# Kernel tuning notes

Measured on AMD Instinct MI355X. Metric: run time of the kernel, lower is better.

## Reference

```python
import jax, jax.numpy as jnp
import numpy as np

RARITY_ALPHA = 0.5


def _forward(obs_emb, observed_mask, lengths, avg_interval, var_prior_emb_tensor,
             rarity_W, adjI, p2s_W1, p2s_b1, p2s_W2, p2s_b2,
             Wu, bu, Wr, br, Wc, bc):
    B, T, N, D = obs_emb.shape
    I = jnp.eye(N, dtype=obs_emb.dtype)
    # hypernetwork conditioning vector per node (prior_to_state MLP); identical
    # across batch since var_prior_emb_tensor is repeated over the batch dim.
    vv = jax.nn.relu(var_prior_emb_tensor @ p2s_W1 + p2s_b1) @ p2s_W2 + p2s_b2  # [N,E]
    vv = jnp.broadcast_to(vv[None], (B, N, vv.shape[-1]))                        # [B,N,E]
    tot = observed_mask.sum(axis=1)  # var_total_obs [B,N]

    def gate(z, W, b):
        # MLP_Param: per-node weights W_n = sum_e vv[n,e]*W[e]; fused einsum avoids
        # materializing [B,N,2D+1,D].
        return jnp.einsum('bni,bne,eio->bno', z, vv, W) + jnp.einsum('bne,eo->bno', vv, b)

    def step_fn(carry, xs):
        h, out = carry
        cur_obs, m, cur_avg, step = xs  # [B,N,D], [B,N], [B,N], scalar
        rs = RARITY_ALPHA * jnp.tanh(cur_avg / (tot + 1.0))                  # [B,N]
        rmat = -rarity_W * jnp.abs(rs[:, :, None] - rs[:, None, :])          # [B,N,N]
        # adj_mask[b,i,j] = observed(b,i)*observed(b,j)  (column-set then row-zero)
        adj_mask = m[:, :, None] * m[:, None, :]
        cur_adj = adjI * (1.0 + rmat) * adj_mask * (1.0 - I) + I             # [B,N,N]
        x = jnp.concatenate([cur_obs, rs[..., None]], axis=-1)              # [B,N,D+1]
        comb = jnp.einsum('bij,bjf->bif', cur_adj,
                          jnp.concatenate([x, h], axis=-1))                  # [B,N,2D+1]
        r = jax.nn.sigmoid(gate(comb, Wr, br))
        u = jax.nn.sigmoid(gate(comb, Wu, bu))
        mm = m[..., None] > 0
        h1 = jnp.where(mm, r * h, h)                      # h[nodes_ind] = r*h[nodes_ind]
        cand = jnp.tanh(gate(jnp.concatenate([x, h1], axis=-1), Wc, bc))
        h2 = jnp.where(mm, (1.0 - u) * h1 + u * cand, h1)  # scatter back at observed nodes
        out = jnp.where((step == lengths - 1)[:, None, None], h2, out)
        return (h2, out), None

    h0 = jnp.zeros((B, N, D), obs_emb.dtype)
    xs = (obs_emb.transpose(1, 0, 2, 3), observed_mask.transpose(1, 0, 2),
          avg_interval.transpose(1, 0, 2), jnp.arange(T))
    (_, out), _ = jax.lax.scan(step_fn, (h0, jnp.zeros_like(h0)), xs)
    return out


def setup_inputs() -> dict:
    B, T, N, D, E = 32, 64, 128, 64, 5
    key = jax.random.key(0)
    ks = jax.random.split(key, 18)
    inp = {}
    inp['obs_emb'] = jax.random.normal(ks[0], (B, T, N, D), jnp.float32)
    inp['adj'] = jax.random.normal(ks[1], (N, N), jnp.float32)  # unused by forward
    inp['observed_mask'] = (jax.random.uniform(ks[2], (B, T, N)) < 0.5).astype(jnp.float32)
    inp['observed_tp'] = jax.random.uniform(ks[3], (B, T), jnp.float32)       # unused
    inp['tp_emb_tensor'] = jax.random.normal(ks[4], (B, T, 1), jnp.float32)   # unused
    inp['lengths'] = jax.random.randint(ks[5], (B,), T // 2, T + 1, jnp.int32)
    inp['avg_interval'] = jax.random.uniform(ks[6], (B, T, N), jnp.float32)
    inp['var_prior_emb_tensor'] = jax.random.normal(ks[7], (N, 768), jnp.float32)
    # learned parameters
    inp['rarity_W'] = jax.random.normal(ks[8], (N, N), jnp.float32)
    inp['adjI'] = jnp.eye(N, dtype=jnp.float32) + 0.01 * jax.random.normal(ks[9], (N, N), jnp.float32)
    inp['p2s_W1'] = 0.05 * jax.random.normal(ks[10], (768, 2 * D), jnp.float32)
    inp['p2s_b1'] = jnp.zeros((2 * D,), jnp.float32)
    inp['p2s_W2'] = 0.1 * jax.random.normal(ks[11], (2 * D, E), jnp.float32)
    inp['p2s_b2'] = jnp.zeros((E,), jnp.float32)
    inp['Wu'] = 0.1 * jax.random.normal(ks[12], (E, 2 * D + 1, D), jnp.float32)
    inp['bu'] = 0.1 * jax.random.normal(ks[13], (E, D), jnp.float32)
    inp['Wr'] = 0.1 * jax.random.normal(ks[14], (E, 2 * D + 1, D), jnp.float32)
    inp['br'] = 0.1 * jax.random.normal(ks[15], (E, D), jnp.float32)
    inp['Wc'] = 0.1 * jax.random.normal(ks[16], (E, 2 * D + 1, D), jnp.float32)
    inp['bc'] = 0.1 * jax.random.normal(ks[17], (E, D), jnp.float32)
    return inp


def reference(obs_emb, adj, observed_mask, observed_tp, tp_emb_tensor, lengths,
              avg_interval, var_prior_emb_tensor, rarity_W, adjI, p2s_W1, p2s_b1,
              p2s_W2, p2s_b2, Wu, bu, Wr, br, Wc, bc):
    # adj, observed_tp, tp_emb_tensor are accepted but never used, as in the torch code
    return _forward(obs_emb, observed_mask, lengths, avg_interval, var_prior_emb_tensor,
                    rarity_W, adjI, p2s_W1, p2s_b1, p2s_W2, p2s_b2,
                    Wu, bu, Wr, br, Wc, bc)
```

## Files before the change

### kernel.cpp

```cpp
#include <hip/hip_runtime.h>
#include <math.h>

constexpr size_t WS_VV  = 1024;
constexpr size_t WS_TOT = 2048;
constexpr size_t WS_RS  = 8192;
constexpr size_t WS_WH  = 270336;
constexpr size_t WS_WX  = 1843200;
constexpr size_t WS_BF  = 3440640;
constexpr size_t WS_H   = 3465216;
constexpr size_t WS_CH  = 3727360;
constexpr size_t WS_CX  = 3989504;
constexpr size_t WS_GXR = 8249344;
constexpr size_t WS_GXU = 12443648;
constexpr size_t WS_CXC = 16637952;

__device__ __forceinline__ float sigm(float x){ return 1.f/(1.f+expf(-x)); }

__device__ __forceinline__ float2 ld2_mall(const float* p){
  union { unsigned long long u; float2 f; } cv;
  cv.u = __hip_atomic_load((const unsigned long long*)p, __ATOMIC_RELAXED,
                           __HIP_MEMORY_SCOPE_AGENT);
  return cv.f;
}
__device__ __forceinline__ void st2_mall(float* p, float a, float b){
  union { unsigned long long u; float2 f; } cv;
  cv.f = make_float2(a, b);
  __hip_atomic_store((unsigned long long*)p, cv.u, __ATOMIC_RELAXED,
                     __HIP_MEMORY_SCOPE_AGENT);
}

__global__ void k_vv(const float* __restrict__ vpe, const float* __restrict__ W1,
                     const float* __restrict__ b1, const float* __restrict__ W2,
                     const float* __restrict__ b2, float* __restrict__ ws){
  int n = blockIdx.x, tid = threadIdx.x;
  __shared__ float hid[128];
  if (tid < 128){
    float acc = b1[tid];
    for (int k=0;k<768;k++) acc = fmaf(vpe[n*768+k], W1[k*128+tid], acc);
    hid[tid] = fmaxf(acc, 0.f);
  }
  __syncthreads();
  if (tid < 5){
    float acc = b2[tid];
    for (int h=0;h<128;h++) acc = fmaf(hid[h], W2[h*5+tid], acc);
    ws[WS_VV + n*5 + tid] = acc;
  }
}

__global__ void k_fold(const float* __restrict__ Wr, const float* __restrict__ Wu,
                       const float* __restrict__ Wc, const float* __restrict__ br,
                       const float* __restrict__ bu, const float* __restrict__ bc,
                       float* __restrict__ ws){
  int bid = blockIdx.x; int g = bid>>7; int n = bid&127;
  const float* W  = (g==0)?Wr:(g==1)?Wu:Wc;
  const float* bb = (g==0)?br:(g==1)?bu:bc;
  float v[5];
#pragma unroll
  for (int e=0;e<5;e++) v[e] = ws[WS_VV + n*5 + e];
  for (int idx=threadIdx.x; idx<129*64; idx+=256){
    int i = idx>>6, o = idx&63;
    float a = 0.f;
#pragma unroll
    for (int e=0;e<5;e++) a = fmaf(v[e], W[(e*129+i)*64+o], a);
    if (i < 65) ws[WS_WX + (size_t)(g*128+n)*4160 + i*64 + o] = a;
    else        ws[WS_WH + (size_t)(g*128+n)*4096 + (i-65)*64 + o] = a;
  }
  if (threadIdx.x < 64){
    int o = threadIdx.x; float a = 0.f;
#pragma unroll
    for (int e=0;e<5;e++) a = fmaf(v[e], bb[e*64+o], a);
    ws[WS_BF + (g*128+n)*64 + o] = a;
  }
}

__global__ void k_tot(const float* __restrict__ mask, float* __restrict__ ws){
  int id = blockIdx.x*256 + threadIdx.x;
  int b = id>>7, n = id&127;
  float s = 0.f;
  for (int t=0;t<64;t++) s += mask[(b*64+t)*128 + n];
  ws[WS_TOT + b*128 + n] = s;
}

__global__ void k_rs(const float* __restrict__ avg, float* __restrict__ ws){
  int id = blockIdx.x*256 + threadIdx.x;
  int b = id>>13, n = id&127;
  float tot = ws[WS_TOT + b*128 + n];
  ws[WS_RS + id] = 0.5f * tanhf(avg[id] / (tot + 1.f));
}

__global__ __launch_bounds__(256) void p4a(const float* __restrict__ obs,
      const float* __restrict__ mask, const float* __restrict__ adjI,
      const float* __restrict__ rW, const int* __restrict__ lengths,
      float* __restrict__ ws, int c0){
  int rc = blockIdx.x;
  int b = rc>>4, tl = rc&15, t = c0 + tl;
  if (t >= lengths[b]) return;
  int rt = b*64 + t;
  __shared__ float xt[64*68];
  __shared__ float adjh[128*68];
  __shared__ float rs_l[128], m_l[128];
  int tid = threadIdx.x;
  if (tid < 128){ rs_l[tid] = ws[WS_RS + rt*128 + tid]; m_l[tid] = mask[rt*128 + tid]; }
  __syncthreads();
  int it = tid>>3, ft = tid&7, i0 = it*4, f0 = ft*8;
  float4 aL[4], aH[4]; float a64[4];
#pragma unroll
  for (int ii=0;ii<4;ii++){ aL[ii]=make_float4(0,0,0,0); aH[ii]=make_float4(0,0,0,0); a64[ii]=0.f; }
  for (int half=0; half<2; half++){
    __syncthreads();
    int j0 = half*64;
    for (int idx=tid; idx<4096; idx+=256){
      int jl = idx>>6, f = idx&63;
      xt[jl*68+f] = obs[(size_t)rt*8192 + (j0+jl)*64 + f];
    }
    if (tid < 64) xt[tid*68+64] = rs_l[j0+tid];
    for (int idx=tid; idx<8192; idx+=256){
      int i = idx>>6, jl = idx&63, j = j0+jl;
      float a;
      if (i == j) a = 1.f;
      else {
        int gi = i*128 + j;
        float dd = fabsf(rs_l[i] - rs_l[j]);
        a = adjI[gi] * (1.f - rW[gi]*dd) * m_l[i] * m_l[j];
      }
      adjh[i*68+jl] = a;
    }
    __syncthreads();
    for (int jb=0; jb<16; jb++){
      float4 av[4];
#pragma unroll
      for (int ii=0;ii<4;ii++) av[ii] = *(const float4*)&adjh[(i0+ii)*68 + jb*4];
#pragma unroll
      for (int jj=0;jj<4;jj++){
        int jl = jb*4 + jj;
        float4 xlo = *(const float4*)&xt[jl*68 + f0];
        float4 xhi = *(const float4*)&xt[jl*68 + f0 + 4];
        float xr = xt[jl*68 + 64];
#pragma unroll
        for (int ii=0;ii<4;ii++){
          float a = (jj==0)?av[ii].x:(jj==1)?av[ii].y:(jj==2)?av[ii].z:av[ii].w;
          aL[ii].x = fmaf(a, xlo.x, aL[ii].x); aL[ii].y = fmaf(a, xlo.y, aL[ii].y);
          aL[ii].z = fmaf(a, xlo.z, aL[ii].z); aL[ii].w = fmaf(a, xlo.w, aL[ii].w);
          aH[ii].x = fmaf(a, xhi.x, aH[ii].x); aH[ii].y = fmaf(a, xhi.y, aH[ii].y);
          aH[ii].z = fmaf(a, xhi.z, aH[ii].z); aH[ii].w = fmaf(a, xhi.w, aH[ii].w);
          a64[ii] = fmaf(a, xr, a64[ii]);
        }
      }
    }
  }
#pragma unroll
  for (int ii=0;ii<4;ii++){
    int i = i0 + ii;
    size_t base = WS_CX + (size_t)i*33280 + (size_t)rc*65 + f0;
    ws[base+0]=aL[ii].x; ws[base+1]=aL[ii].y; ws[base+2]=aL[ii].z; ws[base+3]=aL[ii].w;
    ws[base+4]=aH[ii].x; ws[base+5]=aH[ii].y; ws[base+6]=aH[ii].z; ws[base+7]=aH[ii].w;
    if (ft == 0) ws[WS_CX + (size_t)i*33280 + (size_t)rc*65 + 64] = a64[ii];
  }
}

__global__ __launch_bounds__(256) void p4b(const float* __restrict__ obs,
      const int* __restrict__ lengths, float* __restrict__ ws, int c0){
  int bid = blockIdx.x;
  int g = bid >> 9; int r2 = bid & 511; int n = r2 >> 2; int tile = r2 & 3;
  __shared__ float A[128*69];
  __shared__ float Wl[65*64];
  __shared__ float bl[64];
  __shared__ int slen[32];
  int tid = threadIdx.x;
  if (tid < 32) slen[tid] = lengths[tid];
  for (int idx=tid; idx<4160; idx+=256) Wl[idx] = ws[WS_WX + (size_t)(g*128+n)*4160 + idx];
  if (tid < 64) bl[tid] = ws[WS_BF + (g*128+n)*64 + tid];
  if (g < 2){
    const float* src = &ws[WS_CX + (size_t)n*33280 + (size_t)tile*8320];
    for (int idx=tid; idx<8320; idx+=256){
      int r = idx/65, f = idx - r*65;
      A[r*69+f] = src[idx];
    }
  } else {
    for (int idx=tid; idx<8320; idx+=256){
      int r = idx/65, f = idx - r*65;
      int grow = tile*128 + r;
      int gb = grow>>4, t = c0 + (grow&15);
      float v = (f < 64) ? obs[(size_t)(gb*64+t)*8192 + n*64 + f]
                         : ws[WS_RS + (gb*64+t)*128 + n];
      A[r*69+f] = v;
    }
  }
  __syncthreads();
  int rt8 = tid>>4, dq = tid&15;
  float4 acc[8];
#pragma unroll
  for (int rr=0;rr<8;rr++) acc[rr] = make_float4(0,0,0,0);
  for (int k=0;k<65;k++){
    float4 w = *(const float4*)&Wl[k*64 + dq*4];
#pragma unroll
    for (int rr=0;rr<8;rr++){
      float a = A[(rt8*8+rr)*69 + k];
      acc[rr].x = fmaf(a,w.x,acc[rr].x); acc[rr].y = fmaf(a,w.y,acc[rr].y);
      acc[rr].z = fmaf(a,w.z,acc[rr].z); acc[rr].w = fmaf(a,w.w,acc[rr].w);
    }
  }
  float4 b4 = *(const float4*)&bl[dq*4];
  float* dst = &ws[(g==0)?WS_GXR:(g==1)?WS_GXU:WS_CXC];
#pragma unroll
  for (int rr=0;rr<8;rr++){
    int grow = tile*128 + rt8*8 + rr;
    int gb = grow>>4, gtl = grow&15;
    if (c0 + gtl < slen[gb]){
      float4 o; o.x=acc[rr].x+b4.x; o.y=acc[rr].y+b4.y; o.z=acc[rr].z+b4.z; o.w=acc[rr].w+b4.w;
      *(float4*)&dst[((size_t)(n*16+gtl)*32 + gb)*64 + dq*4] = o;
    }
  }
}

__global__ __launch_bounds__(256) void krec(const float* __restrict__ mask,
      const int* __restrict__ lengths, const float* __restrict__ adjI,
      const float* __restrict__ rWm, float* __restrict__ out, float* __restrict__ ws,
      int c0){
  unsigned* hfl = (unsigned*)ws;
  const int bid = blockIdx.x, tid = threadIdx.x;
  const int bA = bid>>3, s = bid&7, ns = s*16;
  __shared__ float hs[8192];
  __shared__ float adjT[2560];
  __shared__ float chT[1088];
  __shared__ float hT[1088];
  __shared__ float rs_l[128], m_l[128];
  const int lenA = lengths[bA];
  const int ng = tid>>6, fA = tid&63;
  const int nl = tid>>4, fq = tid&15;
  const int n  = ns + nl;
  float* hbuf = &ws[WS_H];
  const float* wrg = &ws[WS_WH + (size_t)(0*128+n)*4096];
  const float* wug = &ws[WS_WH + (size_t)(1*128+n)*4096];
  const float* wcg = &ws[WS_WH + (size_t)(2*128+n)*4096];

  for (int t=c0; t<c0+16; t++){
    if (t >= lenA){
      if (tid == 0)
        __hip_atomic_store(&hfl[bid], (unsigned)(t+1), __ATOMIC_RELAXED,
                           __HIP_MEMORY_SCOPE_AGENT);
      __syncthreads();
      continue;
    }
    if (tid < 128) rs_l[tid] = ws[WS_RS + (size_t)(bA*64+t)*128 + tid];
    else           m_l[tid-128] = mask[(size_t)(bA*64+t)*128 + (tid-128)];
    __syncthreads();
    for (int idx=tid; idx<2048; idx+=256){
      int j = idx&127, il = idx>>7, I = ns+il;
      float a;
      if (I == j) a = 1.f;
      else {
        int gi = I*128 + j;
        float dd = fabsf(rs_l[I] - rs_l[j]);
        a = adjI[gi]*(1.f - rWm[gi]*dd)*m_l[I]*m_l[j];
      }
      adjT[j*20 + il] = a;
    }
    const int tl = t - c0;
    size_t gof = ((size_t)(n*16+tl)*32 + bA)*64 + fq*4;
    float4 arv = *(const float4*)&ws[WS_GXR + gof];
    float4 auv = *(const float4*)&ws[WS_GXU + gof];
    float4 acv = *(const float4*)&ws[WS_CXC + gof];
    float  msv = m_l[n];
    if (t > 0){
      if (tid < 8){
        unsigned tgt = (unsigned)t; int guard = 0;
        while (__hip_atomic_load(&hfl[bA*8 + tid], __ATOMIC_RELAXED,
                 __HIP_MEMORY_SCOPE_AGENT) < tgt && ++guard < (1<<20))
          __builtin_amdgcn_s_sleep(2);
      }
    }
    __syncthreads();
#pragma unroll
    for (int k=0;k<16;k++){
      int p = tid + 256*k;
      float2 v = ld2_mall(&hbuf[(size_t)bA*8192 + 2*p]);
      *(float2*)&hs[2*p] = v;
    }
    __syncthreads();
    float acc[4] = {0.f,0.f,0.f,0.f};
#pragma unroll 4
    for (int j=0;j<128;j++){
      float hv = hs[j*64 + fA];
      float4 a4 = *(const float4*)&adjT[j*20 + ng*4];
      acc[0] = fmaf(a4.x, hv, acc[0]);
      acc[1] = fmaf(a4.y, hv, acc[1]);
      acc[2] = fmaf(a4.z, hv, acc[2]);
      acc[3] = fmaf(a4.w, hv, acc[3]);
    }
#pragma unroll
    for (int r=0;r<4;r++) chT[(ng*4+r)*68 + fA] = acc[r];
    __syncthreads();
#pragma unroll 4
    for (int k=0;k<64;k++){
      float cv = chT[nl*68 + k];
      float4 wr4 = *(const float4*)&wrg[k*64 + fq*4];
      float4 wu4 = *(const float4*)&wug[k*64 + fq*4];
      arv.x = fmaf(cv,wr4.x,arv.x); arv.y = fmaf(cv,wr4.y,arv.y);
      arv.z = fmaf(cv,wr4.z,arv.z); arv.w = fmaf(cv,wr4.w,arv.w);
      auv.x = fmaf(cv,wu4.x,auv.x); auv.y = fmaf(cv,wu4.y,auv.y);
      auv.z = fmaf(cv,wu4.z,auv.z); auv.w = fmaf(cv,wu4.w,auv.w);
    }
    float4 rr4, uu4, h1;
    rr4.x = sigm(arv.x); rr4.y = sigm(arv.y); rr4.z = sigm(arv.z); rr4.w = sigm(arv.w);
    uu4.x = sigm(auv.x); uu4.y = sigm(auv.y); uu4.z = sigm(auv.z); uu4.w = sigm(auv.w);
    float4 hown = *(const float4*)&hs[n*64 + fq*4];
    bool ob = msv > 0.f;
    h1.x = ob ? rr4.x*hown.x : hown.x;
    h1.y = ob ? rr4.y*hown.y : hown.y;
    h1.z = ob ? rr4.z*hown.z : hown.z;
    h1.w = ob ? rr4.w*hown.w : hown.w;
    *(float4*)&hT[nl*68 + fq*4] = h1;
    __syncthreads();
#pragma unroll 4
    for (int k=0;k<64;k++){
      float hv1 = hT[nl*68 + k];
      float4 wc4 = *(const float4*)&wcg[k*64 + fq*4];
      acv.x = fmaf(hv1,wc4.x,acv.x); acv.y = fmaf(hv1,wc4.y,acv.y);
      acv.z = fmaf(hv1,wc4.z,acv.z); acv.w = fmaf(hv1,wc4.w,acv.w);
    }
    float4 cd, h2;
    cd.x = tanhf(acv.x); cd.y = tanhf(acv.y); cd.z = tanhf(acv.z); cd.w = tanhf(acv.w);
    h2.x = ob ? (1.f-uu4.x)*h1.x + uu4.x*cd.x : h1.x;
    h2.y = ob ? (1.f-uu4.y)*h1.y + uu4.y*cd.y : h1.y;
    h2.z = ob ? (1.f-uu4.z)*h1.z + uu4.z*cd.z : h1.z;
    h2.w = ob ? (1.f-uu4.w)*h1.w + uu4.w*cd.w : h1.w;
    float* hp = &hbuf[((size_t)bA*128 + n)*64 + fq*4];
    st2_mall(hp,   h2.x, h2.y);
    st2_mall(hp+2, h2.z, h2.w);
    if (t == lenA-1)
      *(float4*)&out[((size_t)bA*128 + n)*64 + fq*4] = h2;
    __syncthreads();
    asm volatile("s_waitcnt vmcnt(0)" ::: "memory");
    if (tid == 0)
      __hip_atomic_store(&hfl[bid], (unsigned)(t+1), __ATOMIC_RELAXED,
                         __HIP_MEMORY_SCOPE_AGENT);
  }
}

extern "C" void kernel_launch(void* const* d_in, const int* in_sizes, int n_in,
                              void* d_out, int out_size, void* d_ws, size_t ws_size,
                              hipStream_t stream){
  const float* obs  = (const float*)d_in[0];
  const float* maskp= (const float*)d_in[2];
  const int*   lens = (const int*)d_in[5];
  const float* avg  = (const float*)d_in[6];
  const float* vpe  = (const float*)d_in[7];
  const float* rW   = (const float*)d_in[8];
  const float* adjI = (const float*)d_in[9];
  const float* W1   = (const float*)d_in[10];
  const float* b1   = (const float*)d_in[11];
  const float* W2   = (const float*)d_in[12];
  const float* b2   = (const float*)d_in[13];
  const float* Wu   = (const float*)d_in[14];
  const float* bu   = (const float*)d_in[15];
  const float* Wr   = (const float*)d_in[16];
  const float* br   = (const float*)d_in[17];
  const float* Wc   = (const float*)d_in[18];
  const float* bc   = (const float*)d_in[19];
  float* out = (float*)d_out;
  float* ws  = (float*)d_ws;
  hipMemsetAsync(d_ws, 0, 4096, stream);
  hipMemsetAsync((char*)d_ws + WS_H*sizeof(float), 0, 262144*sizeof(float), stream);
  k_vv  <<<128, 256, 0, stream>>>(vpe, W1, b1, W2, b2, ws);
  k_fold<<<384, 256, 0, stream>>>(Wr, Wu, Wc, br, bu, bc, ws);
  k_tot <<<16,  256, 0, stream>>>(maskp, ws);
  k_rs  <<<1024,256, 0, stream>>>(avg, ws);
  for (int c = 0; c < 4; c++){
    int c0 = c*16;
    p4a <<<512, 256, 0, stream>>>(obs, maskp, adjI, rW, lens, ws, c0);
    p4b <<<1536,256, 0, stream>>>(obs, lens, ws, c0);
    krec<<<256, 256, 0, stream>>>(maskp, lens, adjI, rW, out, ws, c0);
  }
}
```

Before: 1.528 ms.

## Split recurrent step into batch-major aggregation and node-major gate phases

```diff
diff --git a/kernel.cpp b/kernel.cpp
--- a/kernel.cpp
+++ b/kernel.cpp
@@ -217,123 +217,157 @@
       const int* __restrict__ lengths, const float* __restrict__ adjI,
       const float* __restrict__ rWm, float* __restrict__ out, float* __restrict__ ws,
       int c0){
-  unsigned* hfl = (unsigned*)ws;
+  unsigned* cfl = (unsigned*)ws;
+  unsigned* hfl = ((unsigned*)ws) + 256;
   const int bid = blockIdx.x, tid = threadIdx.x;
-  const int bA = bid>>3, s = bid&7, ns = s*16;
+  const int bA = bid>>3, sA = bid&7, ns = sA*16;
+  const int nB = bid>>1, hf = bid&1, b0 = hf*16;
   __shared__ float hs[8192];
   __shared__ float adjT[2560];
-  __shared__ float chT[1088];
+  __shared__ float cT[1088];
   __shared__ float hT[1088];
   __shared__ float rs_l[128], m_l[128];
   const int lenA = lengths[bA];
-  const int ng = tid>>6, fA = tid&63;
-  const int nl = tid>>4, fq = tid&15;
-  const int n  = ns + nl;
+  const int il = tid>>4, fq = tid&15;
+  const int bb = b0 + il;
+  const int slenB = lengths[bb];
   float* hbuf = &ws[WS_H];
-  const float* wrg = &ws[WS_WH + (size_t)(0*128+n)*4096];
-  const float* wug = &ws[WS_WH + (size_t)(1*128+n)*4096];
-  const float* wcg = &ws[WS_WH + (size_t)(2*128+n)*4096];
+  float* chb  = &ws[WS_CH];
+  const float* wrg = &ws[WS_WH + (size_t)(0*128+nB)*4096];
+  const float* wug = &ws[WS_WH + (size_t)(1*128+nB)*4096];
+  const float* wcg = &ws[WS_WH + (size_t)(2*128+nB)*4096];
+  float4 hst;
+  { const float* hp = &hbuf[((size_t)bb*128+nB)*64 + fq*4];
+    float2 lo = ld2_mall(hp), hi = ld2_mall(hp+2);
+    hst = make_float4(lo.x, lo.y, hi.x, hi.y); }
 
   for (int t=c0; t<c0+16; t++){
-    if (t >= lenA){
-      if (tid == 0)
-        __hip_atomic_store(&hfl[bid], (unsigned)(t+1), __ATOMIC_RELAXED,
-                           __HIP_MEMORY_SCOPE_AGENT);
-      __syncthreads();
-      continue;
-    }
-    if (tid < 128) rs_l[tid] = ws[WS_RS + (size_t)(bA*64+t)*128 + tid];
-    else           m_l[tid-128] = mask[(size_t)(bA*64+t)*128 + (tid-128)];
-    __syncthreads();
-    for (int idx=tid; idx<2048; idx+=256){
-      int j = idx&127, il = idx>>7, I = ns+il;
-      float a;
-      if (I == j) a = 1.f;
-      else {
-        int gi = I*128 + j;
-        float dd = fabsf(rs_l[I] - rs_l[j]);
-        a = adjI[gi]*(1.f - rWm[gi]*dd)*m_l[I]*m_l[j];
-      }
-      adjT[j*20 + il] = a;
-    }
     const int tl = t - c0;
-    size_t gof = ((size_t)(n*16+tl)*32 + bA)*64 + fq*4;
-    float4 arv = *(const float4*)&ws[WS_GXR + gof];
-    float4 auv = *(const float4*)&ws[WS_GXU + gof];
-    float4 acv = *(const float4*)&ws[WS_CXC + gof];
-    float  msv = m_l[n];
-    if (t > 0){
-      if (tid < 8){
-        unsigned tgt = (unsigned)t; int guard = 0;
-        while (__hip_atomic_load(&hfl[bA*8 + tid], __ATOMIC_RELAXED,
-                 __HIP_MEMORY_SCOPE_AGENT) < tgt && ++guard < (1<<20))
-          __builtin_amdgcn_s_sleep(2);
-      }
-    }
-    __syncthreads();
-#pragma unroll
-    for (int k=0;k<16;k++){
-      int p = tid + 256*k;
-      float2 v = ld2_mall(&hbuf[(size_t)bA*8192 + 2*p]);
-      *(float2*)&hs[2*p] = v;
-    }
-    __syncthreads();
-    float acc[4] = {0.f,0.f,0.f,0.f};
+    const bool aliveA = (t < lenA);
+    const bool aliveB = (t < slenB);
+    if (aliveA){
+      if (tid < 128) rs_l[tid] = ws[WS_RS + (size_t)(bA*64+t)*128 + tid];
+      else           m_l[tid-128] = mask[(size_t)(bA*64+t)*128 + (tid-128)];
+    }
+    __syncthreads();
+    if (aliveA){
+      for (int idx=tid; idx<2048; idx+=256){
+        int j = idx&127, r = idx>>7, I = ns+r;
+        float a;
+        if (I == j) a = 1.f;
+        else {
+          int gi = I*128 + j;
+          float dd = fabsf(rs_l[I] - rs_l[j]);
+          a = adjI[gi]*(1.f - rWm[gi]*dd)*m_l[I]*m_l[j];
+        }
+        adjT[j*20 + r] = a;
+      }
+    }
+    float4 arv, auv, acv; float msv = 0.f;
+    if (aliveB){
+      size_t gof = ((size_t)(nB*16+tl)*32 + bb)*64 + fq*4;
+      arv = *(const float4*)&ws[WS_GXR + gof];
+      auv = *(const float4*)&ws[WS_GXU + gof];
+      acv = *(const float4*)&ws[WS_CXC + gof];
+      msv = mask[(size_t)(bb*64+t)*128 + nB];
+    }
+    if (aliveA && t > 0 && tid < 128){
+      unsigned tgt = (unsigned)t; int guard = 0;
+      while (__hip_atomic_load(&hfl[tid*2 + (bA>>4)], __ATOMIC_RELAXED,
+               __HIP_MEMORY_SCOPE_AGENT) < tgt && ++guard < (1<<20))
+        __builtin_amdgcn_s_sleep(1);
+    }
+    __syncthreads();
+    if (aliveA){
+#pragma unroll
+      for (int k2=0;k2<16;k2++){
+        int p = tid + 256*k2;
+        float2 v = ld2_mall(&hbuf[(size_t)bA*8192 + 2*p]);
+        *(float2*)&hs[2*p] = v;
+      }
+    }
+    __syncthreads();
+    if (aliveA && tid < 128){
+      int pr = tid>>4;
+      float4 a0 = make_float4(0,0,0,0), a1 = a0;
 #pragma unroll 4
-    for (int j=0;j<128;j++){
-      float hv = hs[j*64 + fA];
-      float4 a4 = *(const float4*)&adjT[j*20 + ng*4];
-      acc[0] = fmaf(a4.x, hv, acc[0]);
-      acc[1] = fmaf(a4.y, hv, acc[1]);
-      acc[2] = fmaf(a4.z, hv, acc[2]);
-      acc[3] = fmaf(a4.w, hv, acc[3]);
-    }
-#pragma unroll
-    for (int r=0;r<4;r++) chT[(ng*4+r)*68 + fA] = acc[r];
-    __syncthreads();
+      for (int j=0;j<128;j++){
+        float2 aj = *(const float2*)&adjT[j*20 + pr*2];
+        float4 h4 = *(const float4*)&hs[j*64 + fq*4];
+        a0.x = fmaf(aj.x,h4.x,a0.x); a0.y = fmaf(aj.x,h4.y,a0.y);
+        a0.z = fmaf(aj.x,h4.z,a0.z); a0.w = fmaf(aj.x,h4.w,a0.w);
+        a1.x = fmaf(aj.y,h4.x,a1.x); a1.y = fmaf(aj.y,h4.y,a1.y);
+        a1.z = fmaf(aj.y,h4.z,a1.z); a1.w = fmaf(aj.y,h4.w,a1.w);
+      }
+      float* cp0 = &chb[((size_t)bA*128 + ns + pr*2)*64 + fq*4];
+      st2_mall(cp0,    a0.x, a0.y); st2_mall(cp0+2,  a0.z, a0.w);
+      st2_mall(cp0+64, a1.x, a1.y); st2_mall(cp0+66, a1.z, a1.w);
+    }
+    __syncthreads();
+    if (tid == 0)
+      __hip_atomic_store(&cfl[sA*32 + bA], (unsigned)(t+1), __ATOMIC_RELAXED,
+                         __HIP_MEMORY_SCOPE_AGENT);
+    if (aliveB && fq == 0){
+      unsigned tgt = (unsigned)(t+1); int guard = 0;
+      while (__hip_atomic_load(&cfl[(nB>>4)*32 + bb], __ATOMIC_RELAXED,
+               __HIP_MEMORY_SCOPE_AGENT) < tgt && ++guard < (1<<20))
+        __builtin_amdgcn_s_sleep(1);
+    }
+    __syncthreads();
+    if (aliveB){
+      const float* cp = &chb[((size_t)bb*128 + nB)*64 + fq*4];
+      float2 u = ld2_mall(cp), v = ld2_mall(cp+2);
+      cT[il*68 + fq*4    ] = u.x; cT[il*68 + fq*4 + 1] = u.y;
+      cT[il*68 + fq*4 + 2] = v.x; cT[il*68 + fq*4 + 3] = v.y;
+    }
+    __syncthreads();
+    float4 uu, h1v;
+    const bool ob = msv > 0.f;
+    if (aliveB){
 #pragma unroll 4
-    for (int k=0;k<64;k++){
-      float cv = chT[nl*68 + k];
-      float4 wr4 = *(const float4*)&wrg[k*64 + fq*4];
-      float4 wu4 = *(const float4*)&wug[k*64 + fq*4];
-      arv.x = fmaf(cv,wr4.x,arv.x); arv.y = fmaf(cv,wr4.y,arv.y);
-      arv.z = fmaf(cv,wr4.z,arv.z); arv.w = fmaf(cv,wr4.w,arv.w);
-      auv.x = fmaf(cv,wu4.x,auv.x); auv.y = fmaf(cv,wu4.y,auv.y);
-      auv.z = fmaf(cv,wu4.z,auv.z); auv.w = fmaf(cv,wu4.w,auv.w);
-    }
-    float4 rr4, uu4, h1;
-    rr4.x = sigm(arv.x); rr4.y = sigm(arv.y); rr4.z = sigm(arv.z); rr4.w = sigm(arv.w);
-    uu4.x = sigm(auv.x); uu4.y = sigm(auv.y); uu4.z = sigm(auv.z); uu4.w = sigm(auv.w);
-    float4 hown = *(const float4*)&hs[n*64 + fq*4];
-    bool ob = msv > 0.f;
-    h1.x = ob ? rr4.x*hown.x : hown.x;
-    h1.y = ob ? rr4.y*hown.y : hown.y;
-    h1.z = ob ? rr4.z*hown.z : hown.z;
-    h1.w = ob ? rr4.w*hown.w : hown.w;
-    *(float4*)&hT[nl*68 + fq*4] = h1;
-    __syncthreads();
+      for (int k=0;k<64;k++){
+        float cv = cT[il*68 + k];
+        float4 wr4 = *(const float4*)&wrg[k*64 + fq*4];
+        float4 wu4 = *(const float4*)&wug[k*64 + fq*4];
+        arv.x = fmaf(cv,wr4.x,arv.x); arv.y = fmaf(cv,wr4.y,arv.y);
+        arv.z = fmaf(cv,wr4.z,arv.z); arv.w = fmaf(cv,wr4.w,arv.w);
+        auv.x = fmaf(cv,wu4.x,auv.x); auv.y = fmaf(cv,wu4.y,auv.y);
+        auv.z = fmaf(cv,wu4.z,auv.z); auv.w = fmaf(cv,wu4.w,auv.w);
+      }
+      float4 rr;
+      rr.x = sigm(arv.x); rr.y = sigm(arv.y); rr.z = sigm(arv.z); rr.w = sigm(arv.w);
+      uu.x = sigm(auv.x); uu.y = sigm(auv.y); uu.z = sigm(auv.z); uu.w = sigm(auv.w);
+      h1v.x = ob ? rr.x*hst.x : hst.x;
+      h1v.y = ob ? rr.y*hst.y : hst.y;
+      h1v.z = ob ? rr.z*hst.z : hst.z;
+      h1v.w = ob ? rr.w*hst.w : hst.w;
+      *(float4*)&hT[il*68 + fq*4] = h1v;
+    }
+    __syncthreads();
+    if (aliveB){
 #pragma unroll 4
-    for (int k=0;k<64;k++){
-      float hv1 = hT[nl*68 + k];
-      float4 wc4 = *(const float4*)&wcg[k*64 + fq*4];
-      acv.x = fmaf(hv1,wc4.x,acv.x); acv.y = fmaf(hv1,wc4.y,acv.y);
-      acv.z = fmaf(hv1,wc4.z,acv.z); acv.w = fmaf(hv1,wc4.w,acv.w);
-    }
-    float4 cd, h2;
-    cd.x = tanhf(acv.x); cd.y = tanhf(acv.y); cd.z = tanhf(acv.z); cd.w = tanhf(acv.w);
-    h2.x = ob ? (1.f-uu4.x)*h1.x + uu4.x*cd.x : h1.x;
-    h2.y = ob ? (1.f-uu4.y)*h1.y + uu4.y*cd.y : h1.y;
-    h2.z = ob ? (1.f-uu4.z)*h1.z + uu4.z*cd.z : h1.z;
-    h2.w = ob ? (1.f-uu4.w)*h1.w + uu4.w*cd.w : h1.w;
-    float* hp = &hbuf[((size_t)bA*128 + n)*64 + fq*4];
-    st2_mall(hp,   h2.x, h2.y);
-    st2_mall(hp+2, h2.z, h2.w);
-    if (t == lenA-1)
-      *(float4*)&out[((size_t)bA*128 + n)*64 + fq*4] = h2;
-    __syncthreads();
-    asm volatile("s_waitcnt vmcnt(0)" ::: "memory");
+      for (int k=0;k<64;k++){
+        float hv = hT[il*68 + k];
+        float4 wc4 = *(const float4*)&wcg[k*64 + fq*4];
+        acv.x = fmaf(hv,wc4.x,acv.x); acv.y = fmaf(hv,wc4.y,acv.y);
+        acv.z = fmaf(hv,wc4.z,acv.z); acv.w = fmaf(hv,wc4.w,acv.w);
+      }
+      float4 cd, h2;
+      cd.x = tanhf(acv.x); cd.y = tanhf(acv.y); cd.z = tanhf(acv.z); cd.w = tanhf(acv.w);
+      h2.x = ob ? (1.f-uu.x)*h1v.x + uu.x*cd.x : h1v.x;
+      h2.y = ob ? (1.f-uu.y)*h1v.y + uu.y*cd.y : h1v.y;
+      h2.z = ob ? (1.f-uu.z)*h1v.z + uu.z*cd.z : h1v.z;
+      h2.w = ob ? (1.f-uu.w)*h1v.w + uu.w*cd.w : h1v.w;
+      hst = h2;
+      float* hp = &hbuf[((size_t)bb*128 + nB)*64 + fq*4];
+      st2_mall(hp,   h2.x, h2.y);
+      st2_mall(hp+2, h2.z, h2.w);
+      if (t == slenB-1)
+        *(float4*)&out[((size_t)bb*128 + nB)*64 + fq*4] = h2;
+    }
+    __syncthreads();
     if (tid == 0)
-      __hip_atomic_store(&hfl[bid], (unsigned)(t+1), __ATOMIC_RELAXED,
+      __hip_atomic_store(&hfl[nB*2 + hf], (unsigned)(t+1), __ATOMIC_RELAXED,
                          __HIP_MEMORY_SCOPE_AGENT);
   }
 }
```

New measurement: 1.675 ms. 1.1x slower.
